# Performance work log

Measured on AMD Instinct MI355X. Metric: run time of the kernel, lower is better.

Reference implementation:

```python
import jax, jax.numpy as jnp
import numpy as np

B, E, D, NH, NP = 4, 32, 1024, 16, 4
LQ = E * E
DH = D // NH


def layer_norm(x, g, b, eps=1e-6):
    m = x.mean(-1, keepdims=True)
    v = ((x - m) ** 2).mean(-1, keepdims=True)
    return (x - m) / jnp.sqrt(v + eps) * g + b


def get_ref(H, W):
    # matches MSCrossAttnBlock.get_reference_points: centers normalized to [0,1], (x, y) order
    ys, xs = jnp.meshgrid((jnp.arange(H, dtype=jnp.float32) + 0.5) / H,
                          (jnp.arange(W, dtype=jnp.float32) + 0.5) / W, indexing='ij')
    return jnp.stack([xs.ravel(), ys.ravel()], -1)  # (H*W, 2)


def bilinear_sample(value_l, loc, H, W):
    # value_l: (N, nH, H*W, dh); loc: (N, Lq, nH, P, 2) normalized to [0,1]
    # replicates F.grid_sample(align_corners=False, padding_mode='zeros') with grid = 2*loc - 1
    N, Lq, nH, P, _ = loc.shape
    x = loc[..., 0] * W - 0.5
    y = loc[..., 1] * H - 0.5
    x0 = jnp.floor(x)
    y0 = jnp.floor(y)
    wx1 = x - x0
    wy1 = y - y0
    out = 0.0
    for dy, wy in ((0, 1.0 - wy1), (1, wy1)):
        for dx, wx in ((0, 1.0 - wx1), (1, wx1)):
            xi = x0 + dx
            yi = y0 + dy
            valid = (xi >= 0) & (xi < W) & (yi >= 0) & (yi < H)
            idx = (jnp.clip(yi, 0, H - 1) * W + jnp.clip(xi, 0, W - 1)).astype(jnp.int32)
            idx_t = idx.transpose(0, 2, 1, 3).reshape(N, nH, Lq * P)  # (N, nH, Lq*P)
            g = jnp.take_along_axis(value_l, idx_t[..., None], axis=2)  # (N, nH, Lq*P, dh)
            g = g.reshape(N, nH, Lq, P, -1).transpose(0, 2, 1, 3, 4)  # (N, Lq, nH, P, dh)
            w = (wx * wy) * valid.astype(value_l.dtype)
            out = out + g * w[..., None]
    return out


def msdeform(query, ref, inp, shapes, Wv, bv, Wo, bo, Wa, ba, Wp, bp):
    # MSDeformAttn forward (no padding mask)
    N, Lq, d = query.shape
    nL = len(shapes)
    value = (inp @ Wv.T + bv).reshape(N, -1, NH, DH).transpose(0, 2, 1, 3)  # (N, nH, Lin, dh)
    off = (query @ Wo.T + bo).reshape(N, Lq, NH, nL, NP, 2)
    attw = jax.nn.softmax((query @ Wa.T + ba).reshape(N, Lq, NH, nL * NP), axis=-1)
    attw = attw.reshape(N, Lq, NH, nL, NP)
    normalizer = jnp.array([[w, h] for (h, w) in shapes], dtype=query.dtype)  # (nL, 2) = [W, H]
    loc = ref[None, :, None, None, None, :] + off / normalizer[None, None, None, :, None, :]
    out = 0.0
    start = 0
    for l, (H, W) in enumerate(shapes):
        sampled = bilinear_sample(value[:, :, start:start + H * W], loc[:, :, :, l], H, W)
        out = out + (sampled * attw[:, :, :, l, :, None]).sum(3)  # (N, Lq, nH, dh)
        start += H * W
    return out.reshape(N, Lq, d) @ Wp.T + bp


def setup_inputs() -> dict:
    key = jax.random.key(0)
    ks = iter(jax.random.split(key, 64))
    def rnd(shape, scale):
        return jax.random.normal(next(ks), shape, dtype=jnp.float32) * scale
    inp = {}
    for i in range(4):
        inp[f'src{i}'] = rnd((B, LQ, D), 1.0)
    for nm in ('qn', 'fn', 'n1'):
        inp[nm + '_g'] = jnp.ones((D,), jnp.float32)
        inp[nm + '_b'] = jnp.zeros((D,), jnp.float32)
    inp['gamma1'] = rnd((D,), 0.1)
    inp['gamma2'] = rnd((D,), 0.1)
    ws = D ** -0.5
    for pre, nl in (('ca', 4), ('sa', 1)):
        inp[pre + '_vw'] = rnd((D, D), ws)
        inp[pre + '_vb'] = jnp.zeros((D,), jnp.float32)
        inp[pre + '_ow'] = rnd((NH * nl * NP * 2, D), ws)
        inp[pre + '_ob'] = rnd((NH * nl * NP * 2,), 0.1)
        inp[pre + '_aw'] = rnd((NH * nl * NP, D), ws)
        inp[pre + '_ab'] = jnp.zeros((NH * nl * NP,), jnp.float32)
        inp[pre + '_pw'] = rnd((D, D), ws)
        inp[pre + '_pb'] = jnp.zeros((D,), jnp.float32)
    return inp


def reference(src0, src1, src2, src3, qn_g, qn_b, fn_g, fn_b, n1_g, n1_b, gamma1, gamma2,
              ca_vw, ca_vb, ca_ow, ca_ob, ca_aw, ca_ab, ca_pw, ca_pb,
              sa_vw, sa_vb, sa_ow, sa_ob, sa_aw, sa_ab, sa_pw, sa_pb):
    shapes4 = [(E, E)] * 4
    feat = jnp.concatenate([src0, src1, src2, src3], axis=1)  # (B, 4*LQ, D)
    query = src3  # srcs[-1], pos embed is None
    ref = get_ref(E, E)  # (LQ, 2)
    attn = msdeform(layer_norm(query, qn_g, qn_b), ref, layer_norm(feat, fn_g, fn_b),
                    shapes4, ca_vw, ca_vb, ca_ow, ca_ob, ca_aw, ca_ab, ca_pw, ca_pb)
    attn1 = layer_norm(attn, n1_g, n1_b)
    attn2 = msdeform(attn1, ref, attn1, [(E, E)],
                     sa_vw, sa_vb, sa_ow, sa_ob, sa_aw, sa_ab, sa_pw, sa_pb)
    attn = attn + gamma2 * attn2
    return query + gamma1 * attn
```

## Files before the change

### kernel.cpp

```cpp
#include <hip/hip_runtime.h>


#define DEV __device__ __forceinline__

typedef float f32x4 __attribute__((ext_vector_type(4)));
typedef __bf16 bf16x8 __attribute__((ext_vector_type(8)));

DEV unsigned short f2bf(float f) {
  union { float f; unsigned u; } a; a.f = f;
  unsigned r = a.u + 0x7fffu + ((a.u >> 16) & 1u);
  return (unsigned short)(r >> 16);
}
DEV float bf2f(unsigned short h) {
  union { unsigned u; float f; } a; a.u = ((unsigned)h) << 16;
  return a.f;
}

DEV void gl_lds16(const unsigned short* g, unsigned short* l) {
  __builtin_amdgcn_global_load_lds(
      (const __attribute__((address_space(1))) void*)g,
      (__attribute__((address_space(3))) void*)l, 16, 0, 0);
}

struct CvtArgs {
  const float* src[8];
  unsigned short* dst;
  int off4[9];
};

__global__ __launch_bounds__(256) void f2bf_multi(CvtArgs a) {
  int i = blockIdx.x * 256 + threadIdx.x;
  int seg = 0;
  #pragma unroll
  for (int s = 1; s < 8; ++s) seg += (i >= a.off4[s]) ? 1 : 0;
  const float4 v = ((const float4*)a.src[seg])[i - a.off4[seg]];
  unsigned short* o = a.dst + (size_t)i * 4;
  o[0] = f2bf(v.x); o[1] = f2bf(v.y); o[2] = f2bf(v.z); o[3] = f2bf(v.w);
}

DEV void ln_row_wave(const float* __restrict__ xr, const float* __restrict__ g,
                     const float* __restrict__ b,
                     unsigned short* __restrict__ op_row) {
  const int lane = threadIdx.x & 63;
  float4 v[4];
  float s = 0.f, s2 = 0.f;
  #pragma unroll
  for (int j = 0; j < 4; ++j) {
    v[j] = ((const float4*)xr)[lane + 64 * j];
    s  += v[j].x + v[j].y + v[j].z + v[j].w;
    s2 += v[j].x*v[j].x + v[j].y*v[j].y + v[j].z*v[j].z + v[j].w*v[j].w;
  }
  #pragma unroll
  for (int o = 32; o; o >>= 1) { s += __shfl_xor(s, o); s2 += __shfl_xor(s2, o); }
  const float mean = s * (1.f / 1024.f);
  const float rstd = rsqrtf(s2 * (1.f / 1024.f) - mean * mean + 1e-6f);
  #pragma unroll
  for (int j = 0; j < 4; ++j) {
    float4 gg = ((const float4*)g)[lane + 64 * j];
    float4 bb = ((const float4*)b)[lane + 64 * j];
    ushort4 r;
    r.x = f2bf((v[j].x - mean) * rstd * gg.x + bb.x);
    r.y = f2bf((v[j].y - mean) * rstd * gg.y + bb.y);
    r.z = f2bf((v[j].z - mean) * rstd * gg.z + bb.z);
    r.w = f2bf((v[j].w - mean) * rstd * gg.w + bb.w);
    ((ushort4*)op_row)[lane + 64 * j] = r;
  }
}

__global__ __launch_bounds__(256) void ln_wave_kernel(
    const float* __restrict__ x, const float* __restrict__ g,
    const float* __restrict__ b, unsigned short* __restrict__ out) {
  int row = blockIdx.x * 4 + (threadIdx.x >> 6);
  ln_row_wave(x + (size_t)row * 1024, g, b, out + (size_t)row * 1024);
}

__global__ __launch_bounds__(256) void ln5_wave_kernel(
    const float* __restrict__ s0, const float* __restrict__ s1,
    const float* __restrict__ s2, const float* __restrict__ s3,
    const float* __restrict__ fg, const float* __restrict__ fb,
    const float* __restrict__ qg, const float* __restrict__ qb,
    unsigned short* __restrict__ f_out, unsigned short* __restrict__ q_out) {
  int row = blockIdx.x * 4 + (threadIdx.x >> 6);
  if (row < 16384) {
    int l = row >> 12, inner = row & 4095;
    const float* srcs[4] = {s0, s1, s2, s3};
    int orow = (inner >> 10) * 4096 + l * 1024 + (inner & 1023);
    ln_row_wave(srcs[l] + (size_t)inner * 1024, fg, fb,
                f_out + (size_t)orow * 1024);
  } else {
    int inner = row - 16384;
    ln_row_wave(s3 + (size_t)inner * 1024, qg, qb,
                q_out + (size_t)inner * 1024);
  }
}

struct GemmP {
  const unsigned short* A; const unsigned short* W;
  void* C; void* C1; void* C2;
  const float* b0; const float* b1; const float* b2;
  const float* src3; const float* g1; const float* g2; const float* attnp;
  int M, N, K, tilesM;
};

template <int BM, int BN, int EPI>
DEV void gemm_body(const GemmP& P, int id, unsigned short* smem) {
  constexpr int WMT = BM / 2, WNT = BN / 2;
  constexpr int MF = WMT / 16, NF = WNT / 16;
  constexpr int PA = BM / 64, PB = BN / 64;
  constexpr int BUF = (BM + BN) * 64;
  const int tid = threadIdx.x;
  const int wave = tid >> 6, lane = tid & 63;
  const int wm = (wave & 1) * WMT, wn = (wave >> 1) * WNT;
  const int m0 = (id % P.tilesM) * BM;
  const int n0 = (id / P.tilesM) * BN;
  const int lq = lane >> 4, lm = lane & 15;
  const int r16 = lane >> 2;
  const int cst = lane & 3;
  const int csrc = cst ^ ((r16 >> 1) & 3);
  const int aslot = lq ^ ((lm >> 1) & 3);

  f32x4 acc[MF][NF] = {};
  const int kTiles = P.K >> 6;

  const unsigned short* gA[PA];
  #pragma unroll
  for (int p = 0; p < PA; ++p) {
    int grow = m0 + (wave + 4 * p) * 16 + r16;
    gA[p] = P.A + (size_t)grow * P.K + csrc * 8;
  }
  const unsigned short* gB[PB];
  #pragma unroll
  for (int p = 0; p < PB; ++p) {
    int grow = min(n0 + (wave + 4 * p) * 16 + r16, P.N - 1);
    gB[p] = P.W + (size_t)grow * P.K + csrc * 8;
  }

  auto stage = [&](int b, int t) {
    unsigned short* bA = smem + b * BUF;
    unsigned short* bB = bA + BM * 64;
    const int k0 = t << 6;
    #pragma unroll
    for (int s = 0; s < 2; ++s) {
      #pragma unroll
      for (int p = 0; p < PA; ++p)
        gl_lds16(gA[p] + k0 + s * 32,
                 bA + s * BM * 32 + (wave + 4 * p) * 512);
      #pragma unroll
      for (int p = 0; p < PB; ++p)
        gl_lds16(gB[p] + k0 + s * 32,
                 bB + s * BN * 32 + (wave + 4 * p) * 512);
    }
  };

  stage(0, 0);
  __syncthreads();
  int cur = 0;
  #pragma unroll 1
  for (int t = 0; t < kTiles; ++t) {
    if (t + 1 < kTiles) stage(cur ^ 1, t + 1);
    const unsigned short* bA = smem + cur * BUF;
    const unsigned short* bB = bA + BM * 64;
    #pragma unroll
    for (int s = 0; s < 2; ++s) {
      bf16x8 af[MF], bfr[NF];
      #pragma unroll
      for (int mi = 0; mi < MF; ++mi)
        af[mi] = *(const bf16x8*)(bA + s * BM * 32 + ((wm >> 4) + mi) * 512 + lm * 32 + aslot * 8);
      #pragma unroll
      for (int ni = 0; ni < NF; ++ni)
        bfr[ni] = *(const bf16x8*)(bB + s * BN * 32 + ((wn >> 4) + ni) * 512 + lm * 32 + aslot * 8);
      #pragma unroll
      for (int mi = 0; mi < MF; ++mi)
        #pragma unroll
        for (int ni = 0; ni < NF; ++ni)
          acc[mi][ni] = __builtin_amdgcn_mfma_f32_16x16x32_bf16(
              af[mi], bfr[ni], acc[mi][ni], 0, 0, 0);
    }
    __syncthreads();
    cur ^= 1;
  }

  #pragma unroll
  for (int mi = 0; mi < MF; ++mi) {
    #pragma unroll
    for (int ni = 0; ni < NF; ++ni) {
      const int col = n0 + wn + ni * 16 + lm;
      #pragma unroll
      for (int r2 = 0; r2 < 4; ++r2) {
        const int row = m0 + wm + mi * 16 + lq * 4 + r2;
        float v = acc[mi][ni][r2];
        if constexpr (EPI == 0) {
          ((float*)P.C)[(size_t)row * 1024 + col] = v + P.b0[col];
        } else if constexpr (EPI == 1) {
          ((unsigned short*)P.C)[(size_t)row * 1024 + col] = f2bf(v + P.b0[col]);
        } else if constexpr (EPI == 2) {
          if (col < 512)
            ((float*)P.C)[(size_t)row * 512 + col] = v + P.b0[col];
          else
            ((float*)P.C1)[(size_t)row * 256 + col - 512] = v + P.b1[col - 512];
        } else if constexpr (EPI == 3) {
          if (col < 1024)
            ((unsigned short*)P.C)[(size_t)row * 1024 + col] = f2bf(v + P.b0[col]);
          else if (col < 1152)
            ((float*)P.C1)[(size_t)row * 128 + col - 1024] = v + P.b1[col - 1024];
          else if (col < 1216)
            ((float*)P.C2)[(size_t)row * 64 + col - 1152] = v + P.b2[col - 1152];
        } else {
          size_t i = (size_t)row * 1024 + col;
          float vv = v + P.b0[col];
          ((float*)P.C)[i] = P.src3[i] + P.g1[col] * (P.attnp[i] + P.g2[col] * vv);
        }
      }
    }
  }
}

template <int BM, int BN, int EPI>
__global__ __launch_bounds__(256) void gemm_v3(GemmP P) {
  extern __shared__ __align__(16) unsigned short smem[];
  gemm_body<BM, BN, EPI>(P, blockIdx.x, smem);
}

template <int BM, int BN>
__global__ __launch_bounds__(256) void gemm_dual(GemmP Pv, GemmP Po, int split) {
  extern __shared__ __align__(16) unsigned short smem[];
  if ((int)blockIdx.x < split)
    gemm_body<BM, BN, 1>(Pv, blockIdx.x, smem);
  else
    gemm_body<BM, BN, 2>(Po, blockIdx.x - split, smem);
}

template <int NLEV>
__global__ __launch_bounds__(256) void ms_sample_fused(
    const unsigned short* __restrict__ value, const float* __restrict__ off,
    const float* __restrict__ logits, unsigned short* __restrict__ out) {
  const int nq = blockIdx.x;
  const int wave = threadIdx.x >> 6, lane = threadIdx.x & 63;
  const int h = (wave << 2) + (lane >> 4);
  const int c = (lane & 15) << 2;
  const int q = nq & 1023, n = nq >> 10;
  const float* offp = off + ((size_t)nq * 16 + h) * (NLEV * 8);
  const float* lgp  = logits + ((size_t)nq * 16 + h) * (NLEV * 4);

  float lg[NLEV * 4];
  #pragma unroll
  for (int i = 0; i < NLEV; ++i) {
    float4 v = ((const float4*)lgp)[i];
    lg[4*i] = v.x; lg[4*i+1] = v.y; lg[4*i+2] = v.z; lg[4*i+3] = v.w;
  }
  float mx = lg[0];
  #pragma unroll
  for (int i = 1; i < NLEV * 4; ++i) mx = fmaxf(mx, lg[i]);
  float ssum = 0.f;
  #pragma unroll
  for (int i = 0; i < NLEV * 4; ++i) { lg[i] = __expf(lg[i] - mx); ssum += lg[i]; }
  const float inv = 1.f / ssum;

  const float fqx = (float)(q & 31), fqy = (float)(q >> 5);
  float a0 = 0.f, a1 = 0.f, a2 = 0.f, a3 = 0.f;

  #pragma unroll
  for (int l = 0; l < NLEV; ++l) {
    const unsigned short* vl =
        value + ((size_t)(n * NLEV + l) << 20) + h * 64 + c;
    #pragma unroll
    for (int p = 0; p < 4; ++p) {
      float2 o2 = ((const float2*)offp)[l * 4 + p];
      float aw = lg[l * 4 + p] * inv;
      float xx = fqx + o2.x, yy = fqy + o2.y;
      float xf = floorf(xx), yf = floorf(yy);
      float fx = xx - xf, fy = yy - yf;
      int ix = (int)xf, iy = (int)yf;
      int ix1 = ix + 1, iy1 = iy + 1;
      float vx0 = ((unsigned)ix  < 32u) ? 1.f : 0.f;
      float vx1 = ((unsigned)ix1 < 32u) ? 1.f : 0.f;
      float vy0 = ((unsigned)iy  < 32u) ? 1.f : 0.f;
      float vy1 = ((unsigned)iy1 < 32u) ? 1.f : 0.f;
      int cx0 = min(max(ix, 0), 31), cx1 = min(max(ix1, 0), 31);
      int cy0 = min(max(iy, 0), 31), cy1 = min(max(iy1, 0), 31);
      float w00 = (1.f - fx) * (1.f - fy) * vx0 * vy0 * aw;
      float w01 = fx * (1.f - fy) * vx1 * vy0 * aw;
      float w10 = (1.f - fx) * fy * vx0 * vy1 * aw;
      float w11 = fx * fy * vx1 * vy1 * aw;
      ushort4 u00 = *(const ushort4*)(vl + ((size_t)(cy0 * 32 + cx0) << 10));
      ushort4 u01 = *(const ushort4*)(vl + ((size_t)(cy0 * 32 + cx1) << 10));
      ushort4 u10 = *(const ushort4*)(vl + ((size_t)(cy1 * 32 + cx0) << 10));
      ushort4 u11 = *(const ushort4*)(vl + ((size_t)(cy1 * 32 + cx1) << 10));
      a0 += w00 * bf2f(u00.x) + w01 * bf2f(u01.x) + w10 * bf2f(u10.x) + w11 * bf2f(u11.x);
      a1 += w00 * bf2f(u00.y) + w01 * bf2f(u01.y) + w10 * bf2f(u10.y) + w11 * bf2f(u11.y);
      a2 += w00 * bf2f(u00.z) + w01 * bf2f(u01.z) + w10 * bf2f(u10.z) + w11 * bf2f(u11.z);
      a3 += w00 * bf2f(u00.w) + w01 * bf2f(u01.w) + w10 * bf2f(u10.w) + w11 * bf2f(u11.w);
    }
  }
  ushort4 r;
  r.x = f2bf(a0); r.y = f2bf(a1); r.z = f2bf(a2); r.w = f2bf(a3);
  *(ushort4*)(out + ((size_t)nq * 16 + h) * 64 + c) = r;
}

extern "C" void kernel_launch(void* const* d_in, const int* in_sizes, int n_in,
                              void* d_out, int out_size, void* d_ws,
                              size_t ws_size, hipStream_t stream) {
  (void)in_sizes; (void)n_in; (void)out_size; (void)ws_size;
  const float* src[4] = {(const float*)d_in[0], (const float*)d_in[1],
                         (const float*)d_in[2], (const float*)d_in[3]};
  const float* qn_g = (const float*)d_in[4];
  const float* qn_b = (const float*)d_in[5];
  const float* fn_g = (const float*)d_in[6];
  const float* fn_b = (const float*)d_in[7];
  const float* n1_g = (const float*)d_in[8];
  const float* n1_b = (const float*)d_in[9];
  const float* gamma1 = (const float*)d_in[10];
  const float* gamma2 = (const float*)d_in[11];
  const float* ca_vw = (const float*)d_in[12];
  const float* ca_vb = (const float*)d_in[13];
  const float* ca_ow = (const float*)d_in[14];
  const float* ca_ob = (const float*)d_in[15];
  const float* ca_aw = (const float*)d_in[16];
  const float* ca_ab = (const float*)d_in[17];
  const float* ca_pw = (const float*)d_in[18];
  const float* ca_pb = (const float*)d_in[19];
  const float* sa_vw = (const float*)d_in[20];
  const float* sa_vb = (const float*)d_in[21];
  const float* sa_ow = (const float*)d_in[22];
  const float* sa_ob = (const float*)d_in[23];
  const float* sa_aw = (const float*)d_in[24];
  const float* sa_ab = (const float*)d_in[25];
  const float* sa_pw = (const float*)d_in[26];
  const float* sa_pb = (const float*)d_in[27];

  char* wsp = (char*)d_ws;
  size_t off = 0;
  auto alloc = [&](size_t bytes) {
    char* r = wsp + off;
    off = (off + bytes + 255) & ~(size_t)255;
    return r;
  };
  const size_t MB = 1024 * 1024;
  unsigned short* w_ca_vw = (unsigned short*)alloc(1024 * 1024 * 2);
  unsigned short* w_ca_ow = (unsigned short*)alloc(512 * 1024 * 2);
  unsigned short* w_ca_aw = (unsigned short*)alloc(256 * 1024 * 2);
  unsigned short* w_ca_pw = (unsigned short*)alloc(1024 * 1024 * 2);
  unsigned short* w_sa_vw = (unsigned short*)alloc(1024 * 1024 * 2);
  unsigned short* w_sa_ow = (unsigned short*)alloc(128 * 1024 * 2);
  unsigned short* w_sa_aw = (unsigned short*)alloc(64 * 1024 * 2);
  unsigned short* w_sa_pw = (unsigned short*)alloc(1024 * 1024 * 2);
  (void)w_ca_aw; (void)w_sa_ow; (void)w_sa_aw;
  char* R1 = alloc(32 * MB);
  char* R2 = alloc(32 * MB);
  char* R3 = alloc(8 * MB);
  char* R4 = alloc(8 * MB);
  char* R5 = alloc(4 * MB);

  unsigned short* f_ln    = (unsigned short*)R1;
  float*          attn    = (float*)R1;
  unsigned short* attn1   = (unsigned short*)(R1 + 16 * MB);
  unsigned short* samp_sa = (unsigned short*)(R1 + 24 * MB);
  unsigned short* val_ca  = (unsigned short*)R2;
  unsigned short* val_sa  = (unsigned short*)R2;
  unsigned short* q_ln    = (unsigned short*)R3;
  unsigned short* samp_ca = (unsigned short*)R3;
  float*          off_ca  = (float*)R4;
  float*          off_sa  = (float*)R4;
  float*          attw_sa = (float*)(R4 + 4 * MB);
  float*          attw_ca = (float*)R5;

  CvtArgs ca;
  ca.src[0] = ca_vw; ca.src[1] = ca_ow; ca.src[2] = ca_aw; ca.src[3] = ca_pw;
  ca.src[4] = sa_vw; ca.src[5] = sa_ow; ca.src[6] = sa_aw; ca.src[7] = sa_pw;
  ca.dst = w_ca_vw;
  const int sizes4[8] = {262144, 131072, 65536, 262144, 262144, 32768, 16384, 262144};
  ca.off4[0] = 0;
  for (int i = 0; i < 8; ++i) ca.off4[i + 1] = ca.off4[i] + sizes4[i];
  f2bf_multi<<<ca.off4[8] / 256, 256, 0, stream>>>(ca);

  ln5_wave_kernel<<<5120, 256, 0, stream>>>(src[0], src[1], src[2], src[3],
                                            fn_g, fn_b, qn_g, qn_b, f_ln, q_ln);

  auto mkP = [](const unsigned short* A, const unsigned short* W, void* C,
                const float* b0, int M, int N, int K, int tilesM) {
    GemmP p{}; p.A = A; p.W = W; p.C = C; p.b0 = b0;
    p.M = M; p.N = N; p.K = K; p.tilesM = tilesM;
    return p;
  };

  constexpr int LDS_128 = 2 * (128 + 128) * 64 * 2;
  constexpr int LDS_64  = 2 * (64 + 128) * 64 * 2;

  {
    GemmP pv = mkP(f_ln, w_ca_vw, val_ca, ca_vb, 16384, 1024, 1024, 128);
    GemmP po = mkP(q_ln, w_ca_ow, off_ca, ca_ob, 4096, 768, 1024, 32);
    po.C1 = attw_ca; po.b1 = ca_ab;
    gemm_dual<128, 128><<<1024 + 192, 256, LDS_128, stream>>>(pv, po, 1024);
  }

  ms_sample_fused<4><<<4096, 256, 0, stream>>>(val_ca, off_ca, attw_ca, samp_ca);
  gemm_v3<64, 128, 0><<<64 * 8, 256, LDS_64, stream>>>(
      mkP(samp_ca, w_ca_pw, attn, ca_pb, 4096, 1024, 1024, 64));

  ln_wave_kernel<<<1024, 256, 0, stream>>>(attn, n1_g, n1_b, attn1);
  {
    GemmP p = mkP(attn1, w_sa_vw, val_sa, sa_vb, 4096, 1216, 1024, 64);
    p.C1 = off_sa; p.b1 = sa_ob; p.C2 = attw_sa; p.b2 = sa_ab;
    gemm_v3<64, 128, 3><<<64 * 10, 256, LDS_64, stream>>>(p);
  }
  ms_sample_fused<1><<<4096, 256, 0, stream>>>(val_sa, off_sa, attw_sa, samp_sa);
  {
    GemmP p = mkP(samp_sa, w_sa_pw, d_out, sa_pb, 4096, 1024, 1024, 64);
    p.src3 = src[3]; p.g1 = gamma1; p.g2 = gamma2; p.attnp = attn;
    gemm_v3<64, 128, 4><<<64 * 8, 256, LDS_64, stream>>>(p);
  }
}
```

Before: 356.5 us.

## Shrink GEMM tiles to 64x64, precompute sampling tables in LDS, fuse convert with layernorm

All GEMMs now use 64x64 tiles, giving more blocks and better CU fill at the cost of less per-block reuse. The deformable sampling kernel computes the softmax, bilinear weights and corner offsets once per (head, point) into shared-memory tables with shuffle reductions, instead of redundantly in every lane. The weight-conversion kernel is merged into the layernorm launch to save one launch. Workspace buffers are no longer aliased, so each intermediate gets its own allocation.

```diff
diff --git a/kernel.cpp b/kernel.cpp
--- a/kernel.cpp
+++ b/kernel.cpp
@@ -28,8 +28,7 @@
   int off4[9];
 };
 
-__global__ __launch_bounds__(256) void f2bf_multi(CvtArgs a) {
-  int i = blockIdx.x * 256 + threadIdx.x;
+DEV void cvt_chunk(const CvtArgs& a, int i) {
   int seg = 0;
   #pragma unroll
   for (int s = 1; s < 8; ++s) seg += (i >= a.off4[s]) ? 1 : 0;
@@ -74,23 +73,28 @@
   ln_row_wave(x + (size_t)row * 1024, g, b, out + (size_t)row * 1024);
 }
 
-__global__ __launch_bounds__(256) void ln5_wave_kernel(
+__global__ __launch_bounds__(256) void cvt_ln5_kernel(
+    CvtArgs a,
     const float* __restrict__ s0, const float* __restrict__ s1,
     const float* __restrict__ s2, const float* __restrict__ s3,
     const float* __restrict__ fg, const float* __restrict__ fb,
     const float* __restrict__ qg, const float* __restrict__ qb,
     unsigned short* __restrict__ f_out, unsigned short* __restrict__ q_out) {
-  int row = blockIdx.x * 4 + (threadIdx.x >> 6);
-  if (row < 16384) {
-    int l = row >> 12, inner = row & 4095;
-    const float* srcs[4] = {s0, s1, s2, s3};
-    int orow = (inner >> 10) * 4096 + l * 1024 + (inner & 1023);
-    ln_row_wave(srcs[l] + (size_t)inner * 1024, fg, fb,
-                f_out + (size_t)orow * 1024);
+  if (blockIdx.x < 5120) {
+    int row = blockIdx.x * 4 + (threadIdx.x >> 6);
+    if (row < 16384) {
+      int l = row >> 12, inner = row & 4095;
+      const float* srcs[4] = {s0, s1, s2, s3};
+      int orow = (inner >> 10) * 4096 + l * 1024 + (inner & 1023);
+      ln_row_wave(srcs[l] + (size_t)inner * 1024, fg, fb,
+                  f_out + (size_t)orow * 1024);
+    } else {
+      int inner = row - 16384;
+      ln_row_wave(s3 + (size_t)inner * 1024, qg, qb,
+                  q_out + (size_t)inner * 1024);
+    }
   } else {
-    int inner = row - 16384;
-    ln_row_wave(s3 + (size_t)inner * 1024, qg, qb,
-                q_out + (size_t)inner * 1024);
+    cvt_chunk(a, (blockIdx.x - 5120) * 256 + threadIdx.x);
   }
 }
 
@@ -221,76 +225,87 @@
   gemm_body<BM, BN, EPI>(P, blockIdx.x, smem);
 }
 
-template <int BM, int BN>
-__global__ __launch_bounds__(256) void gemm_dual(GemmP Pv, GemmP Po, int split) {
+__global__ __launch_bounds__(256) void gemm_dual64(GemmP Pv, GemmP Po, int split) {
   extern __shared__ __align__(16) unsigned short smem[];
   if ((int)blockIdx.x < split)
-    gemm_body<BM, BN, 1>(Pv, blockIdx.x, smem);
+    gemm_body<64, 64, 1>(Pv, blockIdx.x, smem);
   else
-    gemm_body<BM, BN, 2>(Po, blockIdx.x - split, smem);
+    gemm_body<64, 64, 2>(Po, blockIdx.x - split, smem);
 }
 
 template <int NLEV>
 __global__ __launch_bounds__(256) void ms_sample_fused(
     const unsigned short* __restrict__ value, const float* __restrict__ off,
     const float* __restrict__ logits, unsigned short* __restrict__ out) {
+  constexpr int NPTS = NLEV * 4;
+  constexpr int STR = NPTS + 1;
+  __shared__ float4 wTab[16 * STR];
+  __shared__ int2  iTab[16 * STR];
   const int nq = blockIdx.x;
-  const int wave = threadIdx.x >> 6, lane = threadIdx.x & 63;
+  const int tid = threadIdx.x;
+  const int q = nq & 1023, n = nq >> 10;
+
+  if (tid < 16 * NPTS) {
+    const int h1 = tid / NPTS;
+    const int p1 = tid - h1 * NPTS;
+    float lg = logits[((size_t)nq * 16 + h1) * NPTS + p1];
+    float mx = lg;
+    #pragma unroll
+    for (int m = 1; m < NPTS; m <<= 1) mx = fmaxf(mx, __shfl_xor(mx, m));
+    const float e = __expf(lg - mx);
+    float sum = e;
+    #pragma unroll
+    for (int m = 1; m < NPTS; m <<= 1) sum += __shfl_xor(sum, m);
+    const float aw = e / sum;
+    const float2 o2 =
+        ((const float2*)(off + ((size_t)nq * 16 + h1) * NPTS * 2))[p1];
+    const float fqx = (float)(q & 31), fqy = (float)(q >> 5);
+    float xx = fqx + o2.x, yy = fqy + o2.y;
+    float xf = floorf(xx), yf = floorf(yy);
+    float fx = xx - xf, fy = yy - yf;
+    int ix = (int)xf, iy = (int)yf;
+    int ix1 = ix + 1, iy1 = iy + 1;
+    float vx0 = ((unsigned)ix  < 32u) ? 1.f : 0.f;
+    float vx1 = ((unsigned)ix1 < 32u) ? 1.f : 0.f;
+    float vy0 = ((unsigned)iy  < 32u) ? 1.f : 0.f;
+    float vy1 = ((unsigned)iy1 < 32u) ? 1.f : 0.f;
+    int cx0 = min(max(ix, 0), 31), cx1 = min(max(ix1, 0), 31);
+    int cy0 = min(max(iy, 0), 31), cy1 = min(max(iy1, 0), 31);
+    float4 w;
+    w.x = (1.f - fx) * (1.f - fy) * vx0 * vy0 * aw;
+    w.y = fx * (1.f - fy) * vx1 * vy0 * aw;
+    w.z = (1.f - fx) * fy * vx0 * vy1 * aw;
+    w.w = fx * fy * vx1 * vy1 * aw;
+    const int l = p1 >> 2;
+    int2 io;
+    io.x = ((n * NLEV + l) << 20) + ((cy0 * 32 + cx0) << 10);
+    io.y = (cx1 - cx0) | ((cy1 - cy0) << 1);
+    wTab[h1 * STR + p1] = w;
+    iTab[h1 * STR + p1] = io;
+  }
+  __syncthreads();
+
+  const int wave = tid >> 6, lane = tid & 63;
   const int h = (wave << 2) + (lane >> 4);
   const int c = (lane & 15) << 2;
-  const int q = nq & 1023, n = nq >> 10;
-  const float* offp = off + ((size_t)nq * 16 + h) * (NLEV * 8);
-  const float* lgp  = logits + ((size_t)nq * 16 + h) * (NLEV * 4);
-
-  float lg[NLEV * 4];
-  #pragma unroll
-  for (int i = 0; i < NLEV; ++i) {
-    float4 v = ((const float4*)lgp)[i];
-    lg[4*i] = v.x; lg[4*i+1] = v.y; lg[4*i+2] = v.z; lg[4*i+3] = v.w;
-  }
-  float mx = lg[0];
-  #pragma unroll
-  for (int i = 1; i < NLEV * 4; ++i) mx = fmaxf(mx, lg[i]);
-  float ssum = 0.f;
-  #pragma unroll
-  for (int i = 0; i < NLEV * 4; ++i) { lg[i] = __expf(lg[i] - mx); ssum += lg[i]; }
-  const float inv = 1.f / ssum;
-
-  const float fqx = (float)(q & 31), fqy = (float)(q >> 5);
+  const unsigned short* __restrict__ vb = value + h * 64 + c;
   float a0 = 0.f, a1 = 0.f, a2 = 0.f, a3 = 0.f;
 
-  #pragma unroll
-  for (int l = 0; l < NLEV; ++l) {
-    const unsigned short* vl =
-        value + ((size_t)(n * NLEV + l) << 20) + h * 64 + c;
-    #pragma unroll
-    for (int p = 0; p < 4; ++p) {
-      float2 o2 = ((const float2*)offp)[l * 4 + p];
-      float aw = lg[l * 4 + p] * inv;
-      float xx = fqx + o2.x, yy = fqy + o2.y;
-      float xf = floorf(xx), yf = floorf(yy);
-      float fx = xx - xf, fy = yy - yf;
-      int ix = (int)xf, iy = (int)yf;
-      int ix1 = ix + 1, iy1 = iy + 1;
-      float vx0 = ((unsigned)ix  < 32u) ? 1.f : 0.f;
-      float vx1 = ((unsigned)ix1 < 32u) ? 1.f : 0.f;
-      float vy0 = ((unsigned)iy  < 32u) ? 1.f : 0.f;
-      float vy1 = ((unsigned)iy1 < 32u) ? 1.f : 0.f;
-      int cx0 = min(max(ix, 0), 31), cx1 = min(max(ix1, 0), 31);
-      int cy0 = min(max(iy, 0), 31), cy1 = min(max(iy1, 0), 31);
-      float w00 = (1.f - fx) * (1.f - fy) * vx0 * vy0 * aw;
-      float w01 = fx * (1.f - fy) * vx1 * vy0 * aw;
-      float w10 = (1.f - fx) * fy * vx0 * vy1 * aw;
-      float w11 = fx * fy * vx1 * vy1 * aw;
-      ushort4 u00 = *(const ushort4*)(vl + ((size_t)(cy0 * 32 + cx0) << 10));
-      ushort4 u01 = *(const ushort4*)(vl + ((size_t)(cy0 * 32 + cx1) << 10));
-      ushort4 u10 = *(const ushort4*)(vl + ((size_t)(cy1 * 32 + cx0) << 10));
-      ushort4 u11 = *(const ushort4*)(vl + ((size_t)(cy1 * 32 + cx1) << 10));
-      a0 += w00 * bf2f(u00.x) + w01 * bf2f(u01.x) + w10 * bf2f(u10.x) + w11 * bf2f(u11.x);
-      a1 += w00 * bf2f(u00.y) + w01 * bf2f(u01.y) + w10 * bf2f(u10.y) + w11 * bf2f(u11.y);
-      a2 += w00 * bf2f(u00.z) + w01 * bf2f(u01.z) + w10 * bf2f(u10.z) + w11 * bf2f(u11.z);
-      a3 += w00 * bf2f(u00.w) + w01 * bf2f(u01.w) + w10 * bf2f(u10.w) + w11 * bf2f(u11.w);
-    }
+  #pragma unroll 4
+  for (int p = 0; p < NPTS; ++p) {
+    const float4 w = wTab[h * STR + p];
+    const int2 io = iTab[h * STR + p];
+    const unsigned short* b = vb + io.x;
+    const int sx = (io.y & 1) << 10;
+    const int sy = (io.y & 2) << 14;
+    ushort4 u00 = *(const ushort4*)(b);
+    ushort4 u01 = *(const ushort4*)(b + sx);
+    ushort4 u10 = *(const ushort4*)(b + sy);
+    ushort4 u11 = *(const ushort4*)(b + sx + sy);
+    a0 += w.x * bf2f(u00.x) + w.y * bf2f(u01.x) + w.z * bf2f(u10.x) + w.w * bf2f(u11.x);
+    a1 += w.x * bf2f(u00.y) + w.y * bf2f(u01.y) + w.z * bf2f(u10.y) + w.w * bf2f(u11.y);
+    a2 += w.x * bf2f(u00.z) + w.y * bf2f(u01.z) + w.z * bf2f(u10.z) + w.w * bf2f(u11.z);
+    a3 += w.x * bf2f(u00.w) + w.y * bf2f(u01.w) + w.z * bf2f(u10.w) + w.w * bf2f(u11.w);
   }
   ushort4 r;
   r.x = f2bf(a0); r.y = f2bf(a1); r.z = f2bf(a2); r.w = f2bf(a3);
@@ -345,24 +360,18 @@
   unsigned short* w_sa_aw = (unsigned short*)alloc(64 * 1024 * 2);
   unsigned short* w_sa_pw = (unsigned short*)alloc(1024 * 1024 * 2);
   (void)w_ca_aw; (void)w_sa_ow; (void)w_sa_aw;
-  char* R1 = alloc(32 * MB);
-  char* R2 = alloc(32 * MB);
-  char* R3 = alloc(8 * MB);
-  char* R4 = alloc(8 * MB);
-  char* R5 = alloc(4 * MB);
-
-  unsigned short* f_ln    = (unsigned short*)R1;
-  float*          attn    = (float*)R1;
-  unsigned short* attn1   = (unsigned short*)(R1 + 16 * MB);
-  unsigned short* samp_sa = (unsigned short*)(R1 + 24 * MB);
-  unsigned short* val_ca  = (unsigned short*)R2;
-  unsigned short* val_sa  = (unsigned short*)R2;
-  unsigned short* q_ln    = (unsigned short*)R3;
-  unsigned short* samp_ca = (unsigned short*)R3;
-  float*          off_ca  = (float*)R4;
-  float*          off_sa  = (float*)R4;
-  float*          attw_sa = (float*)(R4 + 4 * MB);
-  float*          attw_ca = (float*)R5;
+  unsigned short* f_ln    = (unsigned short*)alloc(32 * MB);
+  unsigned short* q_ln    = (unsigned short*)alloc(8 * MB);
+  unsigned short* val_ca  = (unsigned short*)alloc(32 * MB);
+  float*          off_ca  = (float*)alloc(8 * MB);
+  float*          attw_ca = (float*)alloc(4 * MB);
+  unsigned short* samp_ca = (unsigned short*)alloc(8 * MB);
+  float*          attn    = (float*)alloc(16 * MB);
+  unsigned short* attn1   = (unsigned short*)alloc(8 * MB);
+  unsigned short* val_sa  = (unsigned short*)alloc(8 * MB);
+  float*          off_sa  = (float*)alloc(2 * MB);
+  float*          attw_sa = (float*)alloc(1 * MB);
+  unsigned short* samp_sa = (unsigned short*)alloc(8 * MB);
 
   CvtArgs ca;
   ca.src[0] = ca_vw; ca.src[1] = ca_ow; ca.src[2] = ca_aw; ca.src[3] = ca_pw;
@@ -371,10 +380,8 @@
   const int sizes4[8] = {262144, 131072, 65536, 262144, 262144, 32768, 16384, 262144};
   ca.off4[0] = 0;
   for (int i = 0; i < 8; ++i) ca.off4[i + 1] = ca.off4[i] + sizes4[i];
-  f2bf_multi<<<ca.off4[8] / 256, 256, 0, stream>>>(ca);
-
-  ln5_wave_kernel<<<5120, 256, 0, stream>>>(src[0], src[1], src[2], src[3],
-                                            fn_g, fn_b, qn_g, qn_b, f_ln, q_ln);
+  cvt_ln5_kernel<<<5120 + ca.off4[8] / 256, 256, 0, stream>>>(
+      ca, src[0], src[1], src[2], src[3], fn_g, fn_b, qn_g, qn_b, f_ln, q_ln);
 
   auto mkP = [](const unsigned short* A, const unsigned short* W, void* C,
                 const float* b0, int M, int N, int K, int tilesM) {
@@ -383,30 +390,29 @@
     return p;
   };
 
-  constexpr int LDS_128 = 2 * (128 + 128) * 64 * 2;
-  constexpr int LDS_64  = 2 * (64 + 128) * 64 * 2;
+  constexpr int LDS_6464 = 2 * (64 + 64) * 64 * 2;
 
   {
-    GemmP pv = mkP(f_ln, w_ca_vw, val_ca, ca_vb, 16384, 1024, 1024, 128);
-    GemmP po = mkP(q_ln, w_ca_ow, off_ca, ca_ob, 4096, 768, 1024, 32);
+    GemmP pv = mkP(f_ln, w_ca_vw, val_ca, ca_vb, 16384, 1024, 1024, 256);
+    GemmP po = mkP(q_ln, w_ca_ow, off_ca, ca_ob, 4096, 768, 1024, 64);
     po.C1 = attw_ca; po.b1 = ca_ab;
-    gemm_dual<128, 128><<<1024 + 192, 256, LDS_128, stream>>>(pv, po, 1024);
+    gemm_dual64<<<4096 + 768, 256, LDS_6464, stream>>>(pv, po, 4096);
   }
 
   ms_sample_fused<4><<<4096, 256, 0, stream>>>(val_ca, off_ca, attw_ca, samp_ca);
-  gemm_v3<64, 128, 0><<<64 * 8, 256, LDS_64, stream>>>(
+  gemm_v3<64, 64, 0><<<1024, 256, LDS_6464, stream>>>(
       mkP(samp_ca, w_ca_pw, attn, ca_pb, 4096, 1024, 1024, 64));
 
   ln_wave_kernel<<<1024, 256, 0, stream>>>(attn, n1_g, n1_b, attn1);
   {
     GemmP p = mkP(attn1, w_sa_vw, val_sa, sa_vb, 4096, 1216, 1024, 64);
     p.C1 = off_sa; p.b1 = sa_ob; p.C2 = attw_sa; p.b2 = sa_ab;
-    gemm_v3<64, 128, 3><<<64 * 10, 256, LDS_64, stream>>>(p);
+    gemm_v3<64, 64, 3><<<1216, 256, LDS_6464, stream>>>(p);
   }
   ms_sample_fused<1><<<4096, 256, 0, stream>>>(val_sa, off_sa, attw_sa, samp_sa);
   {
     GemmP p = mkP(samp_sa, w_sa_pw, d_out, sa_pb, 4096, 1024, 1024, 64);
     p.src3 = src[3]; p.g1 = gamma1; p.g2 = gamma2; p.attnp = attn;
-    gemm_v3<64, 128, 4><<<64 * 8, 256, LDS_64, stream>>>(p);
-  }
-}
+    gemm_v3<64, 64, 4><<<1024, 256, LDS_6464, stream>>>(p);
+  }
+}
```

New measurement: 368.0 us. 3.2% more time.
